# Kernel optimization log

Measured on AMD Instinct MI355X. Metric: run time of the kernel, lower is better.

The kernel has to match this reference:

```python
import jax, jax.numpy as jnp
import numpy as np

B, N, H, O = 4096, 32, 64, 32  # batch, input_dim, hidden_dim, output_dim


def setup_inputs() -> dict:
    key = jax.random.key(0)
    ks = jax.random.split(key, 9)
    s = 0.1
    return {
        "x": jax.random.normal(ks[0], (B, N), jnp.float32),
        "phi_w1": jax.random.normal(ks[1], (H, 1), jnp.float32) * s,
        "phi_b1": jax.random.normal(ks[2], (H,), jnp.float32) * s,
        "phi_w2": jax.random.normal(ks[3], (O, H), jnp.float32) * s,
        "phi_b2": jax.random.normal(ks[4], (O,), jnp.float32) * s,
        "psi_w1": jax.random.normal(ks[5], (H, 2 * O), jnp.float32) * s,
        "psi_b1": jax.random.normal(ks[6], (H,), jnp.float32) * s,
        "psi_w2": jax.random.normal(ks[7], (O, H), jnp.float32) * s,
        "psi_b2": jax.random.normal(ks[8], (O,), jnp.float32) * s,
    }


def reference(x, phi_w1, phi_b1, phi_w2, phi_b2, psi_w1, psi_b1, psi_w2, psi_b2):
    n = x.shape[1]
    # phi applied per scalar column, batched: [B, N, H]
    h1 = jax.nn.relu(x[..., None] * phi_w1[:, 0] + phi_b1)
    phi_out = jnp.einsum('bnh,oh->bno', h1, phi_w2) + phi_b2  # [B, N, O]
    # all i<j pairs (static indices)
    ii, jj = np.triu_indices(n, k=1)  # P = n*(n-1)/2
    pairs = jnp.concatenate([phi_out[:, ii], phi_out[:, jj]], axis=-1)  # [B, P, 2O]
    h2 = jax.nn.relu(jnp.einsum('bpt,ht->bph', pairs, psi_w1) + psi_b1)  # [B, P, H]
    psi_out = jnp.einsum('bph,oh->bpo', h2, psi_w2) + psi_b2  # [B, P, O]
    return jnp.sum(psi_out, axis=1)  # [B, O]
```

## Files before the change

kernel.cpp:

```cpp
#include <hip/hip_runtime.h>

namespace {

typedef float v2f  __attribute__((ext_vector_type(2)));
typedef float v4f  __attribute__((ext_vector_type(4)));
typedef float f32x16 __attribute__((ext_vector_type(16)));
typedef short bf16x8 __attribute__((ext_vector_type(8)));
typedef unsigned short ushort;
typedef unsigned short us8 __attribute__((ext_vector_type(8)));
typedef unsigned int v4u __attribute__((ext_vector_type(4)));
typedef __fp16 h2 __attribute__((ext_vector_type(2)));

constexpr int NDIM = 32;
constexpr int HDIM = 64;
constexpr int ODIM = 32;
constexpr float PAIRS = 496.0f;

__device__ __forceinline__ ushort f2bf(float f) {
    unsigned int u = __builtin_bit_cast(unsigned int, f);
    u += 0x7fffu + ((u >> 16) & 1u);
    return (ushort)(u >> 16);
}

__global__ __launch_bounds__(64) void kan_precompute(
    const float* __restrict__ phi_w2, const float* __restrict__ phi_b2,
    const float* __restrict__ psi_w1, const float* __restrict__ psi_b1,
    ushort* __restrict__ Bfrag, float* __restrict__ cconst)
{
    __shared__ float pw2s[32 * 64];
    __shared__ float pw1s[32 * 36];

    const int s = blockIdx.x >> 2, c = blockIdx.x & 3;
    const int lane = threadIdx.x;
    const int hbase = (c & 1) * 32;
    const int off   = (c >> 1) * ODIM;

#pragma unroll
    for (int it = 0; it < 8; ++it) {
        const int idx = it * 256 + lane * 4;
        *(v4f*)&pw2s[idx] = *(const v4f*)(phi_w2 + idx);
    }
#pragma unroll
    for (int it = 0; it < 16; ++it) {
        const int idx = it * 64 + lane;
        const int r = idx >> 5, col = idx & 31;
        pw1s[r * 36 + col] = psi_w1[(hbase + r) * 2 * ODIM + off + col];
    }
    __syncthreads();

    const int row = lane & 31, half = lane >> 5;
    v4f w1r[8];
#pragma unroll
    for (int t = 0; t < 8; ++t) w1r[t] = *(const v4f*)&pw1s[row * 36 + 4 * t];

    us8 out8;
#pragma unroll
    for (int e = 0; e < 8; ++e) {
        const int k = 16 * s + 8 * half + e;
        float m = 0.f;
#pragma unroll
        for (int o = 0; o < 32; ++o)
            m = fmaf(w1r[o >> 2][o & 3], pw2s[o * 64 + k], m);
        out8[e] = f2bf(m);
    }
    *(us8*)(Bfrag + (size_t)(blockIdx.x * 64 + lane) * 8) = out8;

    if (blockIdx.x == 0) {
        float cch = psi_b1[lane];
#pragma unroll
        for (int o = 0; o < ODIM; ++o)
            cch = fmaf(psi_w1[lane * 2 * ODIM + o] + psi_w1[lane * 2 * ODIM + ODIM + o],
                       phi_b2[o], cch);
        cconst[lane] = cch;
    }
}

__global__ __launch_bounds__(256, 4) void kan_main(
    const float* __restrict__ x, const float* __restrict__ phi_w1,
    const float* __restrict__ phi_b1, const float* __restrict__ psi_w2,
    const float* __restrict__ psi_b2, const ushort* __restrict__ Bfrag,
    const float* __restrict__ cconst, float* __restrict__ out)
{
    __shared__ v4u  Blds[1024];
    __shared__ float sred[4][HDIM];

    const int tid  = threadIdx.x;
    const int wave = tid >> 6;
    const int lane = tid & 63;
    const int batch = blockIdx.x * 4 + wave;
    const int row  = lane & 31;
    const int half = lane >> 5;
    const bool hi  = lane >= 32;

    const v4u* gB = (const v4u*)Bfrag;
    const v4u t0 = gB[tid];
    const v4u t1 = gB[tid + 256];
    const v4u t2 = gB[tid + 512];
    const v4u t3 = gB[tid + 768];

    const float xn = x[(size_t)batch * NDIM + row];

    bf16x8 afrag[4];
#pragma unroll
    for (int s = 0; s < 4; ++s) {
        const int kb = 16 * s + 8 * half;
        const v4f w1a = *(const v4f*)(phi_w1 + kb);
        const v4f w1b = *(const v4f*)(phi_w1 + kb + 4);
        const v4f b1a = *(const v4f*)(phi_b1 + kb);
        const v4f b1b = *(const v4f*)(phi_b1 + kb + 4);
        bf16x8 t;
#pragma unroll
        for (int e = 0; e < 4; ++e)
            t[e] = (short)f2bf(fmaxf(fmaf(xn, w1a[e], b1a[e]), 0.f));
#pragma unroll
        for (int e = 0; e < 4; ++e)
            t[4 + e] = (short)f2bf(fmaxf(fmaf(xn, w1b[e], b1b[e]), 0.f));
        afrag[s] = t;
    }

    const float cc0 = cconst[row];
    const float cc1 = cconst[32 + row];

    Blds[tid]       = t0;
    Blds[tid + 256] = t1;
    Blds[tid + 512] = t2;
    Blds[tid + 768] = t3;
    __syncthreads();

    f32x16 acc0, acc1, acc2, acc3;
#pragma unroll
    for (int r = 0; r < 16; ++r) { acc0[r] = cc0; acc1[r] = cc1; acc2[r] = 0.f; acc3[r] = 0.f; }

    const bf16x8* Bf = (const bf16x8*)Blds;
#pragma unroll
    for (int s = 0; s < 4; ++s) {
        const bf16x8 b0 = Bf[(s * 4 + 0) * 64 + lane];
        const bf16x8 b1 = Bf[(s * 4 + 1) * 64 + lane];
        const bf16x8 b2 = Bf[(s * 4 + 2) * 64 + lane];
        const bf16x8 b3 = Bf[(s * 4 + 3) * 64 + lane];
        acc0 = __builtin_amdgcn_mfma_f32_32x32x16_bf16(afrag[s], b0, acc0, 0, 0, 0);
        acc1 = __builtin_amdgcn_mfma_f32_32x32x16_bf16(afrag[s], b1, acc1, 0, 0, 0);
        acc2 = __builtin_amdgcn_mfma_f32_32x32x16_bf16(afrag[s], b2, acc2, 0, 0, 0);
        acc3 = __builtin_amdgcn_mfma_f32_32x32x16_bf16(afrag[s], b3, acc3, 0, 0, 0);
    }

    v2f Ap0[8], Ap1[8], Bp0[8], Bp1[8];
#pragma unroll
    for (int q = 0; q < 8; ++q) {
        v2f own, snd, oth;
        own.x = hi ? acc1[2 * q]     : acc0[2 * q];
        own.y = hi ? acc1[2 * q + 1] : acc0[2 * q + 1];
        snd.x = hi ? acc0[2 * q]     : acc1[2 * q];
        snd.y = hi ? acc0[2 * q + 1] : acc1[2 * q + 1];
        oth.x = __shfl_xor(snd.x, 32);
        oth.y = __shfl_xor(snd.y, 32);
        Ap0[q].x = hi ? oth.x : own.x;  Ap0[q].y = hi ? oth.y : own.y;
        Ap1[q].x = hi ? own.x : oth.x;  Ap1[q].y = hi ? own.y : oth.y;
    }
#pragma unroll
    for (int q = 0; q < 8; ++q) {
        v2f own, snd, oth;
        own.x = hi ? acc3[2 * q]     : acc2[2 * q];
        own.y = hi ? acc3[2 * q + 1] : acc2[2 * q + 1];
        snd.x = hi ? acc2[2 * q]     : acc3[2 * q];
        snd.y = hi ? acc2[2 * q + 1] : acc3[2 * q + 1];
        oth.x = __shfl_xor(snd.x, 32);
        oth.y = __shfl_xor(snd.y, 32);
        Bp0[q].x = hi ? oth.x : own.x;  Bp0[q].y = hi ? oth.y : own.y;
        Bp1[q].x = hi ? own.x : oth.x;  Bp1[q].y = hi ? own.y : oth.y;
    }

    float Af[NDIM], Bn[NDIM];
#pragma unroll
    for (int q = 0; q < 8; ++q) {
        const int n0 = ((2 * q) & 3) + 8 * ((2 * q) >> 2);
        Af[n0]     = Ap0[q].x;  Af[n0 + 1] = Ap0[q].y;
        Af[n0 + 4] = Ap1[q].x;  Af[n0 + 5] = Ap1[q].y;
        Bn[n0]     = Bp0[q].x;  Bn[n0 + 1] = Bp0[q].y;
        Bn[n0 + 4] = Bp1[q].x;  Bn[n0 + 5] = Bp1[q].y;
    }

    h2 Bh[16];
#pragma unroll
    for (int p = 0; p < 16; ++p)
        Bh[p] = __builtin_amdgcn_cvt_pkrtz(Bn[2 * p], Bn[2 * p + 1]);

    const h2 one2  = {(__fp16)1.f, (__fp16)1.f};
    const h2 zero2 = {(__fp16)0.f, (__fp16)0.f};
    float acc[8] = {0.f, 0.f, 0.f, 0.f, 0.f, 0.f, 0.f, 0.f};

#pragma unroll
    for (int t = 0; t < 8; ++t) {
        const h2 ae = __builtin_amdgcn_cvt_pkrtz(Af[4 * t],     Af[4 * t + 2]);
        const h2 bo = __builtin_amdgcn_cvt_pkrtz(Bn[4 * t + 1], Bn[4 * t + 3]);
        const h2 m  = __builtin_elementwise_max(ae + bo, zero2);
        acc[t] = __builtin_amdgcn_fdot2(m, one2, acc[t], false);
    }
#pragma unroll
    for (int i = 0; i < 30; ++i) {
        const h2 ai2 = __builtin_amdgcn_cvt_pkrtz(Af[i], Af[i]);
#pragma unroll
        for (int p = i / 2 + 1; p < 16; ++p) {
            const h2 m = __builtin_elementwise_max(ai2 + Bh[p], zero2);
            acc[p & 7] = __builtin_amdgcn_fdot2(m, one2, acc[p & 7], false);
        }
    }
    const float S = ((acc[0] + acc[1]) + (acc[2] + acc[3])) +
                    ((acc[4] + acc[5]) + (acc[6] + acc[7]));

    sred[wave][lane] = S;

    const int oo = row;
    const float* w2r = psi_w2 + (size_t)oo * HDIM + half * 32;
    float part = 0.f;
#pragma unroll
    for (int r = 0; r < 8; ++r) {
        const v4f w  = *(const v4f*)(w2r + 4 * r);
        const v4f sv = *(const v4f*)&sred[wave][half * 32 + 4 * r];
        part = fmaf(w[0], sv[0], part);
        part = fmaf(w[1], sv[1], part);
        part = fmaf(w[2], sv[2], part);
        part = fmaf(w[3], sv[3], part);
    }
    part += __shfl_down(part, 32);
    if (half == 0)
        out[(size_t)batch * ODIM + oo] = part + PAIRS * psi_b2[oo];
}

}

extern "C" void kernel_launch(void* const* d_in, const int* in_sizes, int n_in,
                              void* d_out, int out_size, void* d_ws, size_t ws_size,
                              hipStream_t stream)
{
    const float* x      = (const float*)d_in[0];
    const float* phi_w1 = (const float*)d_in[1];
    const float* phi_b1 = (const float*)d_in[2];
    const float* phi_w2 = (const float*)d_in[3];
    const float* phi_b2 = (const float*)d_in[4];
    const float* psi_w1 = (const float*)d_in[5];
    const float* psi_b1 = (const float*)d_in[6];
    const float* psi_w2 = (const float*)d_in[7];
    const float* psi_b2 = (const float*)d_in[8];

    ushort* Bfrag = (ushort*)d_ws;
    float* cconst = (float*)((char*)d_ws + 16 * 64 * 8 * sizeof(ushort));
    float* out    = (float*)d_out;

    kan_precompute<<<16, 64, 0, stream>>>(phi_w2, phi_b2, psi_w1, psi_b1, Bfrag, cconst);
    kan_main<<<4096 / 4, 256, 0, stream>>>(x, phi_w1, phi_b1, psi_w2, psi_b2,
                                           Bfrag, cconst, out);
}
```

Measured before the change: 22.18 us.

## Pack MFMA outputs to fp16 before lane exchange and use op_sel splat adds

```diff
diff --git a/kernel.cpp b/kernel.cpp
--- a/kernel.cpp
+++ b/kernel.cpp
@@ -22,6 +22,25 @@
     return (ushort)(u >> 16);
 }
 
+__device__ __forceinline__ unsigned cvt_pk_bf16(float lo, float hi) {
+    unsigned r;
+    asm("v_cvt_pk_bf16_f32 %0, %1, %2" : "=v"(r) : "v"(lo), "v"(hi));
+    return r;
+}
+
+__device__ __forceinline__ h2 padd_splat_lo(h2 a, h2 b) {
+    h2 d;
+    asm("v_pk_add_f16 %0, %1, %2 op_sel:[0,0] op_sel_hi:[0,1]"
+        : "=v"(d) : "v"(a), "v"(b));
+    return d;
+}
+__device__ __forceinline__ h2 padd_splat_hi(h2 a, h2 b) {
+    h2 d;
+    asm("v_pk_add_f16 %0, %1, %2 op_sel:[1,0] op_sel_hi:[1,1]"
+        : "=v"(d) : "v"(a), "v"(b));
+    return d;
+}
+
 __global__ __launch_bounds__(64) void kan_precompute(
     const float* __restrict__ phi_w2, const float* __restrict__ phi_b2,
     const float* __restrict__ psi_w1, const float* __restrict__ psi_b1,
@@ -98,7 +117,9 @@
     const v4u t2 = gB[tid + 512];
     const v4u t3 = gB[tid + 768];
 
-    const float xn = x[(size_t)batch * NDIM + row];
+    const float xn  = x[(size_t)batch * NDIM + row];
+    const float cc0 = cconst[row];
+    const float cc1 = cconst[32 + row];
 
     bf16x8 afrag[4];
 #pragma unroll
@@ -108,18 +129,16 @@
         const v4f w1b = *(const v4f*)(phi_w1 + kb + 4);
         const v4f b1a = *(const v4f*)(phi_b1 + kb);
         const v4f b1b = *(const v4f*)(phi_b1 + kb + 4);
-        bf16x8 t;
-#pragma unroll
-        for (int e = 0; e < 4; ++e)
-            t[e] = (short)f2bf(fmaxf(fmaf(xn, w1a[e], b1a[e]), 0.f));
-#pragma unroll
-        for (int e = 0; e < 4; ++e)
-            t[4 + e] = (short)f2bf(fmaxf(fmaf(xn, w1b[e], b1b[e]), 0.f));
-        afrag[s] = t;
-    }
-
-    const float cc0 = cconst[row];
-    const float cc1 = cconst[32 + row];
+        float h[8];
+#pragma unroll
+        for (int e = 0; e < 4; ++e) h[e]     = fmaxf(fmaf(xn, w1a[e], b1a[e]), 0.f);
+#pragma unroll
+        for (int e = 0; e < 4; ++e) h[4 + e] = fmaxf(fmaf(xn, w1b[e], b1b[e]), 0.f);
+        v4u u;
+#pragma unroll
+        for (int w = 0; w < 4; ++w) u[w] = cvt_pk_bf16(h[2 * w], h[2 * w + 1]);
+        afrag[s] = __builtin_bit_cast(bf16x8, u);
+    }
 
     Blds[tid]       = t0;
     Blds[tid + 256] = t1;
@@ -127,82 +146,78 @@
     Blds[tid + 768] = t3;
     __syncthreads();
 
-    f32x16 acc0, acc1, acc2, acc3;
-#pragma unroll
-    for (int r = 0; r < 16; ++r) { acc0[r] = cc0; acc1[r] = cc1; acc2[r] = 0.f; acc3[r] = 0.f; }
-
     const bf16x8* Bf = (const bf16x8*)Blds;
-#pragma unroll
-    for (int s = 0; s < 4; ++s) {
-        const bf16x8 b0 = Bf[(s * 4 + 0) * 64 + lane];
-        const bf16x8 b1 = Bf[(s * 4 + 1) * 64 + lane];
-        const bf16x8 b2 = Bf[(s * 4 + 2) * 64 + lane];
-        const bf16x8 b3 = Bf[(s * 4 + 3) * 64 + lane];
-        acc0 = __builtin_amdgcn_mfma_f32_32x32x16_bf16(afrag[s], b0, acc0, 0, 0, 0);
-        acc1 = __builtin_amdgcn_mfma_f32_32x32x16_bf16(afrag[s], b1, acc1, 0, 0, 0);
-        acc2 = __builtin_amdgcn_mfma_f32_32x32x16_bf16(afrag[s], b2, acc2, 0, 0, 0);
-        acc3 = __builtin_amdgcn_mfma_f32_32x32x16_bf16(afrag[s], b3, acc3, 0, 0, 0);
-    }
-
-    v2f Ap0[8], Ap1[8], Bp0[8], Bp1[8];
-#pragma unroll
-    for (int q = 0; q < 8; ++q) {
-        v2f own, snd, oth;
-        own.x = hi ? acc1[2 * q]     : acc0[2 * q];
-        own.y = hi ? acc1[2 * q + 1] : acc0[2 * q + 1];
-        snd.x = hi ? acc0[2 * q]     : acc1[2 * q];
-        snd.y = hi ? acc0[2 * q + 1] : acc1[2 * q + 1];
-        oth.x = __shfl_xor(snd.x, 32);
-        oth.y = __shfl_xor(snd.y, 32);
-        Ap0[q].x = hi ? oth.x : own.x;  Ap0[q].y = hi ? oth.y : own.y;
-        Ap1[q].x = hi ? own.x : oth.x;  Ap1[q].y = hi ? own.y : oth.y;
-    }
-#pragma unroll
-    for (int q = 0; q < 8; ++q) {
-        v2f own, snd, oth;
-        own.x = hi ? acc3[2 * q]     : acc2[2 * q];
-        own.y = hi ? acc3[2 * q + 1] : acc2[2 * q + 1];
-        snd.x = hi ? acc2[2 * q]     : acc3[2 * q];
-        snd.y = hi ? acc2[2 * q + 1] : acc3[2 * q + 1];
-        oth.x = __shfl_xor(snd.x, 32);
-        oth.y = __shfl_xor(snd.y, 32);
-        Bp0[q].x = hi ? oth.x : own.x;  Bp0[q].y = hi ? oth.y : own.y;
-        Bp1[q].x = hi ? own.x : oth.x;  Bp1[q].y = hi ? own.y : oth.y;
-    }
-
-    float Af[NDIM], Bn[NDIM];
-#pragma unroll
-    for (int q = 0; q < 8; ++q) {
-        const int n0 = ((2 * q) & 3) + 8 * ((2 * q) >> 2);
-        Af[n0]     = Ap0[q].x;  Af[n0 + 1] = Ap0[q].y;
-        Af[n0 + 4] = Ap1[q].x;  Af[n0 + 5] = Ap1[q].y;
-        Bn[n0]     = Bp0[q].x;  Bn[n0 + 1] = Bp0[q].y;
-        Bn[n0 + 4] = Bp1[q].x;  Bn[n0 + 5] = Bp1[q].y;
-    }
-
-    h2 Bh[16];
-#pragma unroll
-    for (int p = 0; p < 16; ++p)
-        Bh[p] = __builtin_amdgcn_cvt_pkrtz(Bn[2 * p], Bn[2 * p + 1]);
-
+
+    auto exchange = [&](const f32x16& lo32, const f32x16& hi32, h2* outp) {
+#pragma unroll
+        for (int q = 0; q < 8; ++q) {
+            const h2 cl = __builtin_amdgcn_cvt_pkrtz(lo32[2 * q], lo32[2 * q + 1]);
+            const h2 ch = __builtin_amdgcn_cvt_pkrtz(hi32[2 * q], hi32[2 * q + 1]);
+            const h2 own = hi ? ch : cl;
+            const h2 snd = hi ? cl : ch;
+            const unsigned su = __builtin_bit_cast(unsigned, snd);
+            const unsigned ou = (unsigned)__shfl_xor((int)su, 32);
+            const h2 oth = __builtin_bit_cast(h2, ou);
+            const int n0 = ((2 * q) & 3) + 8 * ((2 * q) >> 2);
+            outp[(n0 >> 1)]     = hi ? oth : own;
+            outp[(n0 >> 1) + 2] = hi ? own : oth;
+        }
+    };
+
+    h2 Ah[16], Bh[16];
+    {
+        f32x16 a0, a1;
+#pragma unroll
+        for (int r = 0; r < 16; ++r) { a0[r] = cc0; a1[r] = cc1; }
+#pragma unroll
+        for (int s = 0; s < 4; ++s) {
+            const bf16x8 b0 = Bf[(s * 4 + 0) * 64 + lane];
+            const bf16x8 b1 = Bf[(s * 4 + 1) * 64 + lane];
+            a0 = __builtin_amdgcn_mfma_f32_32x32x16_bf16(afrag[s], b0, a0, 0, 0, 0);
+            a1 = __builtin_amdgcn_mfma_f32_32x32x16_bf16(afrag[s], b1, a1, 0, 0, 0);
+        }
+        exchange(a0, a1, Ah);
+    }
+    {
+        f32x16 a2, a3;
+#pragma unroll
+        for (int r = 0; r < 16; ++r) { a2[r] = 0.f; a3[r] = 0.f; }
+#pragma unroll
+        for (int s = 0; s < 4; ++s) {
+            const bf16x8 b2 = Bf[(s * 4 + 2) * 64 + lane];
+            const bf16x8 b3 = Bf[(s * 4 + 3) * 64 + lane];
+            a2 = __builtin_amdgcn_mfma_f32_32x32x16_bf16(afrag[s], b2, a2, 0, 0, 0);
+            a3 = __builtin_amdgcn_mfma_f32_32x32x16_bf16(afrag[s], b3, a3, 0, 0, 0);
+        }
+        exchange(a2, a3, Bh);
+    }
+
+    const h2 zero2 = {(__fp16)0.f, (__fp16)0.f};
     const h2 one2  = {(__fp16)1.f, (__fp16)1.f};
-    const h2 zero2 = {(__fp16)0.f, (__fp16)0.f};
+    const h2 m01   = {(__fp16)0.f, (__fp16)1.f};
     float acc[8] = {0.f, 0.f, 0.f, 0.f, 0.f, 0.f, 0.f, 0.f};
 
 #pragma unroll
-    for (int t = 0; t < 8; ++t) {
-        const h2 ae = __builtin_amdgcn_cvt_pkrtz(Af[4 * t],     Af[4 * t + 2]);
-        const h2 bo = __builtin_amdgcn_cvt_pkrtz(Bn[4 * t + 1], Bn[4 * t + 3]);
-        const h2 m  = __builtin_elementwise_max(ae + bo, zero2);
-        acc[t] = __builtin_amdgcn_fdot2(m, one2, acc[t], false);
-    }
-#pragma unroll
-    for (int i = 0; i < 30; ++i) {
-        const h2 ai2 = __builtin_amdgcn_cvt_pkrtz(Af[i], Af[i]);
-#pragma unroll
-        for (int p = i / 2 + 1; p < 16; ++p) {
-            const h2 m = __builtin_elementwise_max(ai2 + Bh[p], zero2);
-            acc[p & 7] = __builtin_amdgcn_fdot2(m, one2, acc[p & 7], false);
+    for (int i = 0; i < 31; ++i) {
+        const int m = i >> 1;
+        const h2 ai = Ah[m];
+        if ((i & 1) == 0) {
+            const h2 t = padd_splat_lo(ai, Bh[m]);
+            const h2 r = __builtin_elementwise_max(t, zero2);
+            acc[m & 7] = __builtin_amdgcn_fdot2(r, m01, acc[m & 7], false);
+#pragma unroll
+            for (int p = m + 1; p < 16; ++p) {
+                const h2 tt = padd_splat_lo(ai, Bh[p]);
+                const h2 rr = __builtin_elementwise_max(tt, zero2);
+                acc[p & 7] = __builtin_amdgcn_fdot2(rr, one2, acc[p & 7], false);
+            }
+        } else {
+#pragma unroll
+            for (int p = m + 1; p < 16; ++p) {
+                const h2 tt = padd_splat_hi(ai, Bh[p]);
+                const h2 rr = __builtin_elementwise_max(tt, zero2);
+                acc[p & 7] = __builtin_amdgcn_fdot2(rr, one2, acc[p & 7], false);
+            }
         }
     }
     const float S = ((acc[0] + acc[1]) + (acc[2] + acc[3])) +
```

Result: slower. 22.99 us (+3.6%).
